# Performance work log

Measured on AMD Instinct MI355X. Metric: run time of the kernel, lower is better.

The kernel has to match this reference:

```python
import jax, jax.numpy as jnp
import numpy as np

B = 256
NUM_ROUTES = 1152
NUM_CAPS = 10
D_IN = 8
D_OUT = 16
NUM_ITER = 3
EPS = 1e-5


def setup_inputs() -> dict:
    key = jax.random.key(0)
    k1, k2 = jax.random.split(key)
    u = jax.random.normal(k1, (B, NUM_ROUTES, D_IN), dtype=jnp.float32)
    # learned transform W, torch shape (1, R, C, D_OUT, D_IN) with leading 1 dropped
    W = jax.random.normal(k2, (NUM_ROUTES, NUM_CAPS, D_OUT, D_IN), dtype=jnp.float32)
    return {"u": u, "W": W}


def _squash(x, eps=EPS):
    # In the original, squash sums over the last dim of s_j, which has size 1,
    # so it is effectively elementwise: scale = x^2/(1+x^2), out = scale*x/(|x|+eps)
    sq = x * x
    return sq / (1.0 + sq) * x / (jnp.sqrt(sq) + eps)


def reference(u, W):
    # u_hat[b,r,c,d] = sum_i W[r,c,d,i] * u[b,r,i]   -> (B, R, C, D_OUT)
    u_hat = jnp.einsum('rcdi,bri->brcd', W, u)
    b_ij = jnp.zeros((1, NUM_ROUTES, NUM_CAPS, 1), dtype=u_hat.dtype)
    v = None
    for it in range(NUM_ITER):
        c_ij = jax.nn.softmax(b_ij, axis=1)              # (1, R, C, K), K in {1, D_OUT}
        s = jnp.sum(c_ij * u_hat, axis=1, keepdims=True)  # (B, 1, C, D_OUT)
        v = _squash(s)
        if it < NUM_ITER - 1:
            # a_ij[b,r,c,d] = v[b,0,c,d] * sum_k u_hat[b,r,c,k]  (exact reduction of
            # the original transpose-multiply-sum, avoiding the DxD intermediate)
            a = v * jnp.sum(u_hat, axis=-1, keepdims=True)  # (B, R, C, D_OUT)
            b_ij = b_ij + jnp.mean(a, axis=0, keepdims=True)
    return v.reshape(u.shape[0], NUM_CAPS, D_OUT)
```

## Files before the change

### kernel.cpp

```cpp
#include <hip/hip_runtime.h>
#include <math.h>

#define R_   1152
#define C_   10
#define D_   16
#define I_   8
#define B_   256
#define N_   160
#define K_   9216
#define KS_  32
#define KC_  288

#define OFF_WSUM  0
#define OFF_TT    92160
#define OFF_V     (OFF_TT + 2949120)
#define OFF_BIJ   (OFF_V + 40960)
#define OFF_E     (OFF_BIJ + 184320)
#define OFF_NSA   (OFF_E + 184320)
#define OFF_NSB   (OFF_NSA + 160)
#define OFF_PART  (OFF_NSB + 160)

__device__ __forceinline__ float f4c(const float4 v, int i) {
    return i == 0 ? v.x : i == 1 ? v.y : i == 2 ? v.z : v.w;
}

template <int HASE>
__launch_bounds__(256, 2)
__global__ void gemm_kernel(const float* __restrict__ u, const float* __restrict__ W,
                            const float* __restrict__ E,
                            float* __restrict__ partials, float* __restrict__ Wsum,
                            float* __restrict__ zA, float* __restrict__ zB) {
    int tid = threadIdx.x;
    if (!HASE && blockIdx.x >= 512) {
        int idx = (blockIdx.x - 512) * 256 + tid;
        int r = idx / (C_ * I_);
        int rem = idx % (C_ * I_);
        int c = rem / I_;
        int i = rem % I_;
        const float* p = W + (size_t)r * (C_ * D_ * I_) + c * (D_ * I_) + i;
        float s = 0.0f;
#pragma unroll
        for (int d = 0; d < D_; ++d) s += p[d * I_];
        Wsum[idx] = s;
        return;
    }

    __shared__ float smem[10240];
    int wave = tid >> 6, lane = tid & 63;
    int ng = lane & 15, bg = lane >> 4;
    int bt = blockIdx.x & 15, ks = blockIdx.x >> 4;
    int b0 = bt * 16;
    int n0 = ng * 10;

    if (!HASE && blockIdx.x == 0 && tid < N_) { zA[tid] = 0.0f; zB[tid] = 0.0f; }

    float acc[4][10];
#pragma unroll
    for (int m = 0; m < 4; ++m)
#pragma unroll
        for (int j = 0; j < 10; ++j) acc[m][j] = 0.0f;

    const float* ubase = u + (size_t)(b0 + bg * 4) * K_ + ks * KC_ + wave * 8;

    float4 wr[5];
    float  ee[5];
    float4 uc[8];
    {
        int r = ks * 36 + wave;
#pragma unroll
        for (int it = 0; it < 5; ++it) {
            int idx = it * 64 + lane;
            wr[it] = *(const float4*)(W + (size_t)r * 1280 + idx * 4);
            if (HASE) ee[it] = E[r * N_ + (idx >> 1)];
        }
#pragma unroll
        for (int m = 0; m < 4; ++m)
#pragma unroll
            for (int g = 0; g < 2; ++g)
                uc[m * 2 + g] = *(const float4*)(ubase + (size_t)m * K_ + g * 4);
    }

    int ldsbase = wave * 1280;
    for (int c = 0; c < 9; ++c) {
#pragma unroll
        for (int it = 0; it < 5; ++it) {
            int idx = it * 64 + lane;
            int n = idx >> 1, ih = (idx & 1) * 4;
            float e = HASE ? ee[it] : 1.0f;
            float* q = &smem[ldsbase + ih * 160 + n];
            q[0]   = wr[it].x * e;
            q[160] = wr[it].y * e;
            q[320] = wr[it].z * e;
            q[480] = wr[it].w * e;
        }
        float4 un[8];
        if (c < 8) {
            int r = ks * 36 + (c + 1) * 4 + wave;
#pragma unroll
            for (int it = 0; it < 5; ++it) {
                int idx = it * 64 + lane;
                wr[it] = *(const float4*)(W + (size_t)r * 1280 + idx * 4);
                if (HASE) ee[it] = E[r * N_ + (idx >> 1)];
            }
#pragma unroll
            for (int m = 0; m < 4; ++m)
#pragma unroll
                for (int g = 0; g < 2; ++g)
                    un[m * 2 + g] = *(const float4*)(ubase + (size_t)m * K_ + (c + 1) * 32 + g * 4);
        }
#pragma unroll
        for (int g = 0; g < 2; ++g) {
#pragma unroll
            for (int t4 = 0; t4 < 4; ++t4) {
                const float* wrow = &smem[ldsbase + (g * 4 + t4) * 160 + n0];
                float w[10];
#pragma unroll
                for (int j = 0; j < 10; j += 2) {
                    float2 ww = *(const float2*)(wrow + j);
                    w[j] = ww.x; w[j + 1] = ww.y;
                }
#pragma unroll
                for (int m = 0; m < 4; ++m) {
                    float uav = f4c(uc[m * 2 + g], t4);
#pragma unroll
                    for (int j = 0; j < 10; ++j)
                        acc[m][j] = fmaf(uav, w[j], acc[m][j]);
                }
            }
        }
        if (c < 8) {
#pragma unroll
            for (int q2 = 0; q2 < 8; ++q2) uc[q2] = un[q2];
        }
    }

    __syncthreads();
#pragma unroll
    for (int m = 0; m < 4; ++m)
#pragma unroll
        for (int j = 0; j < 10; ++j)
            smem[wave * 2560 + (bg * 4 + m) * N_ + n0 + j] = acc[m][j];
    __syncthreads();
    float* outp = partials + (size_t)ks * (B_ * N_) + (size_t)b0 * N_;
    for (int f = tid; f < 2560; f += 256)
        outp[f] = smem[f] + smem[2560 + f] + smem[5120 + f] + smem[7680 + f];
}

template <int DOT>
__global__ void rsv_kernel(const float* __restrict__ partials, float* __restrict__ dst,
                           float scale, const float* __restrict__ nsum,
                           const float* __restrict__ u,
                           const float* __restrict__ Wsum, float* __restrict__ tT) {
    int tid = threadIdx.x;
    if (DOT && blockIdx.x >= 160) {
        for (int idx = (blockIdx.x - 160) * 256 + tid; idx < B_ * R_; idx += 512 * 256) {
            int r = idx % R_;
            int b = idx / R_;
            const float4* up = (const float4*)(u + (size_t)idx * I_);
            float4 a0 = up[0], a1 = up[1];
            const float* wp = Wsum + (size_t)r * (C_ * I_);
            float outv[C_];
#pragma unroll
            for (int c = 0; c < C_; ++c) {
                const float4* w4 = (const float4*)(wp + c * I_);
                float4 w0 = w4[0], w1 = w4[1];
                outv[c] = a0.x * w0.x + a0.y * w0.y + a0.z * w0.z + a0.w * w0.w
                        + a1.x * w1.x + a1.y * w1.y + a1.z * w1.z + a1.w * w1.w;
            }
#pragma unroll
            for (int c = 0; c < C_; ++c)
                tT[((size_t)c * B_ + b) * R_ + r] = outv[c];
        }
        return;
    }
    int g = blockIdx.x * 256 + tid;
    float s = 0.0f;
#pragma unroll
    for (int ks = 0; ks < KS_; ++ks) s += partials[(size_t)ks * (B_ * N_) + g];
    if (nsum) s /= nsum[g % N_];
    else      s *= scale;
    float sq = s * s;
    dst[g] = sq / (1.0f + sq) * s / (sqrtf(sq) + 1e-5f);
}

__launch_bounds__(256)
__global__ void bupd_kernel(const float* __restrict__ v, const float* __restrict__ tT,
                            float* __restrict__ bij, float* __restrict__ E,
                            float* __restrict__ nsum, int accumulate) {
    __shared__ float vs[B_ * 16];
    __shared__ float red[16 * 258];
    __shared__ float exs[4][16];
    int tid = threadIdx.x;
    int c = blockIdx.x % 10;
    int r0 = (blockIdx.x / 10) * 16;
    int rsub = tid & 15, bs = tid >> 4;

    for (int q = tid; q < 1024; q += 256) {
        int b = q >> 2, d4 = q & 3;
        ((float4*)vs)[q] = *(const float4*)(v + (size_t)b * N_ + c * 16 + d4 * 4);
    }
    __syncthreads();

    float acc[16];
#pragma unroll
    for (int d = 0; d < 16; ++d) acc[d] = 0.0f;

    const float* tp = tT + ((size_t)c * B_ + bs) * R_ + r0 + rsub;
#pragma unroll
    for (int bb = 0; bb < 16; ++bb) {
        float tv = tp[(size_t)bb * 16 * R_];
        const float4* vrow = (const float4*)(vs + (bb * 16 + bs) * 16);
        float4 v0 = vrow[0], v1 = vrow[1], v2 = vrow[2], v3 = vrow[3];
        acc[0]  = fmaf(tv, v0.x, acc[0]);  acc[1]  = fmaf(tv, v0.y, acc[1]);
        acc[2]  = fmaf(tv, v0.z, acc[2]);  acc[3]  = fmaf(tv, v0.w, acc[3]);
        acc[4]  = fmaf(tv, v1.x, acc[4]);  acc[5]  = fmaf(tv, v1.y, acc[5]);
        acc[6]  = fmaf(tv, v1.z, acc[6]);  acc[7]  = fmaf(tv, v1.w, acc[7]);
        acc[8]  = fmaf(tv, v2.x, acc[8]);  acc[9]  = fmaf(tv, v2.y, acc[9]);
        acc[10] = fmaf(tv, v2.z, acc[10]); acc[11] = fmaf(tv, v2.w, acc[11]);
        acc[12] = fmaf(tv, v3.x, acc[12]); acc[13] = fmaf(tv, v3.y, acc[13]);
        acc[14] = fmaf(tv, v3.z, acc[14]); acc[15] = fmaf(tv, v3.w, acc[15]);
    }
#pragma unroll
    for (int d = 0; d < 16; ++d) red[d * 258 + tid] = acc[d];
    __syncthreads();

    int d = tid & 15, rr = tid >> 4;
    const float* rp = red + d * 258 + rr;
    float s = 0.0f;
#pragma unroll
    for (int q = 0; q < 16; ++q) s += rp[q * 16];
    s *= (1.0f / B_);
    int o = (r0 + rr) * N_ + c * 16 + d;
    if (accumulate) s += bij[o];
    bij[o] = s;
    float ex = __expf(s);
    E[o] = ex;
    ex += __shfl_down(ex, 32, 64);
    ex += __shfl_down(ex, 16, 64);
    int wv = tid >> 6, ln = tid & 63;
    if (ln < 16) exs[wv][ln] = ex;
    __syncthreads();
    if (tid < 16)
        atomicAdd(&nsum[c * 16 + tid],
                  exs[0][tid] + exs[1][tid] + exs[2][tid] + exs[3][tid]);
}

extern "C" void kernel_launch(void* const* d_in, const int* in_sizes, int n_in,
                              void* d_out, int out_size, void* d_ws, size_t ws_size,
                              hipStream_t stream) {
    (void)in_sizes; (void)n_in; (void)out_size; (void)ws_size;
    const float* u = (const float*)d_in[0];
    const float* W = (const float*)d_in[1];
    float* out = (float*)d_out;
    float* ws = (float*)d_ws;

    float* Wsum     = ws + OFF_WSUM;
    float* tT       = ws + OFF_TT;
    float* v        = ws + OFF_V;
    float* bij      = ws + OFF_BIJ;
    float* E        = ws + OFF_E;
    float* nsumA    = ws + OFF_NSA;
    float* nsumB    = ws + OFF_NSB;
    float* partials = ws + OFF_PART;

    gemm_kernel<0><<<872, 256, 0, stream>>>(u, W, nullptr, partials, Wsum, nsumA, nsumB);
    rsv_kernel<1><<<672, 256, 0, stream>>>(partials, v, 1.0f / 1152.0f, nullptr, u, Wsum, tT);
    bupd_kernel<<<720, 256, 0, stream>>>(v, tT, bij, E, nsumA, 0);

    gemm_kernel<1><<<512, 256, 0, stream>>>(u, W, E, partials, nullptr, nullptr, nullptr);
    rsv_kernel<0><<<160, 256, 0, stream>>>(partials, v, 1.0f, nsumA, nullptr, nullptr, nullptr);
    bupd_kernel<<<720, 256, 0, stream>>>(v, tT, bij, E, nsumB, 1);

    gemm_kernel<1><<<512, 256, 0, stream>>>(u, W, E, partials, nullptr, nullptr, nullptr);
    rsv_kernel<0><<<160, 256, 0, stream>>>(partials, out, 1.0f, nsumB, nullptr, nullptr, nullptr);
}
```

Before: 143.9 us.

## Fuse tT computation into gemm extra blocks and squash reduction into bupd

The Wsum computation and the per-(b,r) dot products that build tT move into the extra blocks of the first gemm kernel, which stage the W sums in shared memory. The separate reduce-squash kernels before each b-update are folded into bupd_kernel: each block reduces the split-K partials and squashes v into LDS itself. The launch count drops from 8 to 6 and the Wsum and v round-trips are removed. In exchange, each of 180 bupd blocks now redundantly reduces 32 partial slices for its capsule, and each block covers 64 routes instead of 16, which lowers the grid size.

```diff
diff --git a/kernel.cpp b/kernel.cpp
--- a/kernel.cpp
+++ b/kernel.cpp
@@ -1,5 +1,6 @@
 #include <hip/hip_runtime.h>
 #include <math.h>
+
 
 #define R_   1152
 #define C_   10
@@ -11,10 +12,8 @@
 #define KS_  32
 #define KC_  288
 
-#define OFF_WSUM  0
-#define OFF_TT    92160
-#define OFF_V     (OFF_TT + 2949120)
-#define OFF_BIJ   (OFF_V + 40960)
+#define OFF_TT    0
+#define OFF_BIJ   2949120
 #define OFF_E     (OFF_BIJ + 184320)
 #define OFF_NSA   (OFF_E + 184320)
 #define OFF_NSB   (OFF_NSA + 160)
@@ -28,24 +27,51 @@
 __launch_bounds__(256, 2)
 __global__ void gemm_kernel(const float* __restrict__ u, const float* __restrict__ W,
                             const float* __restrict__ E,
-                            float* __restrict__ partials, float* __restrict__ Wsum,
+                            float* __restrict__ partials, float* __restrict__ tT,
                             float* __restrict__ zA, float* __restrict__ zB) {
     int tid = threadIdx.x;
+    __shared__ float smem[10240];
+
     if (!HASE && blockIdx.x >= 512) {
-        int idx = (blockIdx.x - 512) * 256 + tid;
-        int r = idx / (C_ * I_);
-        int rem = idx % (C_ * I_);
-        int c = rem / I_;
-        int i = rem % I_;
-        const float* p = W + (size_t)r * (C_ * D_ * I_) + c * (D_ * I_) + i;
-        float s = 0.0f;
-#pragma unroll
-        for (int d = 0; d < D_; ++d) s += p[d * I_];
-        Wsum[idx] = s;
+        float* wsl = smem;
+        int r0 = (int)(blockIdx.x - 512) * 16;
+        for (int q = tid; q < 1280; q += 256) {
+            int rr = q / 80, rem = q % 80;
+            const float* p = W + (size_t)(r0 + rr) * 1280 + (rem >> 3) * 128 + (rem & 7);
+            float s = 0.0f;
+#pragma unroll
+            for (int d = 0; d < 16; ++d) s += p[d * 8];
+            wsl[rr * 84 + rem] = s;
+        }
+        __syncthreads();
+        int r = tid & 15, bgrp = tid >> 4;
+        const float* urow = u + (size_t)(r0 + r) * 8;
+        for (int cb = 0; cb < 4; ++cb) {
+            float4 ua[4][2];
+#pragma unroll
+            for (int b4 = 0; b4 < 4; ++b4) {
+                int b = (cb * 4 + b4) * 16 + bgrp;
+                const float4* up = (const float4*)(urow + (size_t)b * K_);
+                ua[b4][0] = up[0]; ua[b4][1] = up[1];
+            }
+#pragma unroll
+            for (int c = 0; c < 10; ++c) {
+                float4 w0 = *(const float4*)&wsl[r * 84 + c * 8];
+                float4 w1 = *(const float4*)&wsl[r * 84 + c * 8 + 4];
+#pragma unroll
+                for (int b4 = 0; b4 < 4; ++b4) {
+                    int b = (cb * 4 + b4) * 16 + bgrp;
+                    float s = ua[b4][0].x * w0.x + ua[b4][0].y * w0.y
+                            + ua[b4][0].z * w0.z + ua[b4][0].w * w0.w
+                            + ua[b4][1].x * w1.x + ua[b4][1].y * w1.y
+                            + ua[b4][1].z * w1.z + ua[b4][1].w * w1.w;
+                    tT[((size_t)c * B_ + b) * R_ + r0 + r] = s;
+                }
+            }
+        }
         return;
     }
 
-    __shared__ float smem[10240];
     int wave = tid >> 6, lane = tid & 63;
     int ng = lane & 15, bg = lane >> 4;
     int bt = blockIdx.x & 15, ks = blockIdx.x >> 4;
@@ -146,70 +172,44 @@
         outp[f] = smem[f] + smem[2560 + f] + smem[5120 + f] + smem[7680 + f];
 }
 
-template <int DOT>
-__global__ void rsv_kernel(const float* __restrict__ partials, float* __restrict__ dst,
-                           float scale, const float* __restrict__ nsum,
-                           const float* __restrict__ u,
-                           const float* __restrict__ Wsum, float* __restrict__ tT) {
-    int tid = threadIdx.x;
-    if (DOT && blockIdx.x >= 160) {
-        for (int idx = (blockIdx.x - 160) * 256 + tid; idx < B_ * R_; idx += 512 * 256) {
-            int r = idx % R_;
-            int b = idx / R_;
-            const float4* up = (const float4*)(u + (size_t)idx * I_);
-            float4 a0 = up[0], a1 = up[1];
-            const float* wp = Wsum + (size_t)r * (C_ * I_);
-            float outv[C_];
-#pragma unroll
-            for (int c = 0; c < C_; ++c) {
-                const float4* w4 = (const float4*)(wp + c * I_);
-                float4 w0 = w4[0], w1 = w4[1];
-                outv[c] = a0.x * w0.x + a0.y * w0.y + a0.z * w0.z + a0.w * w0.w
-                        + a1.x * w1.x + a1.y * w1.y + a1.z * w1.z + a1.w * w1.w;
-            }
-#pragma unroll
-            for (int c = 0; c < C_; ++c)
-                tT[((size_t)c * B_ + b) * R_ + r] = outv[c];
-        }
-        return;
-    }
-    int g = blockIdx.x * 256 + tid;
-    float s = 0.0f;
-#pragma unroll
-    for (int ks = 0; ks < KS_; ++ks) s += partials[(size_t)ks * (B_ * N_) + g];
-    if (nsum) s /= nsum[g % N_];
-    else      s *= scale;
-    float sq = s * s;
-    dst[g] = sq / (1.0f + sq) * s / (sqrtf(sq) + 1e-5f);
-}
-
 __launch_bounds__(256)
-__global__ void bupd_kernel(const float* __restrict__ v, const float* __restrict__ tT,
+__global__ void bupd_kernel(const float* __restrict__ partials, const float* __restrict__ tT,
                             float* __restrict__ bij, float* __restrict__ E,
-                            float* __restrict__ nsum, int accumulate) {
+                            float* __restrict__ nsumOut, const float* __restrict__ nsumIn,
+                            int accumulate) {
     __shared__ float vs[B_ * 16];
     __shared__ float red[16 * 258];
     __shared__ float exs[4][16];
     int tid = threadIdx.x;
     int c = blockIdx.x % 10;
-    int r0 = (blockIdx.x / 10) * 16;
-    int rsub = tid & 15, bs = tid >> 4;
-
-    for (int q = tid; q < 1024; q += 256) {
-        int b = q >> 2, d4 = q & 3;
-        ((float4*)vs)[q] = *(const float4*)(v + (size_t)b * N_ + c * 16 + d4 * 4);
-    }
-    __syncthreads();
-
+    int r0 = (blockIdx.x / 10) * 64;
+
+    {
+        int d = tid & 15, bq = tid >> 4;
+        const float* pp = partials + c * 16 + d;
+        float inv = accumulate ? 1.0f / nsumIn[c * 16 + d] : (1.0f / 1152.0f);
+        for (int bb = 0; bb < 16; ++bb) {
+            int b = bq * 16 + bb;
+            float s = 0.0f;
+#pragma unroll
+            for (int ks = 0; ks < KS_; ++ks) s += pp[(size_t)ks * (B_ * N_) + b * N_];
+            s *= inv;
+            float sq = s * s;
+            vs[b * 16 + d] = sq / (1.0f + sq) * s / (sqrtf(sq) + 1e-5f);
+        }
+    }
+    __syncthreads();
+
+    int rsub = tid & 63, bs = tid >> 6;
     float acc[16];
 #pragma unroll
     for (int d = 0; d < 16; ++d) acc[d] = 0.0f;
 
-    const float* tp = tT + ((size_t)c * B_ + bs) * R_ + r0 + rsub;
-#pragma unroll
-    for (int bb = 0; bb < 16; ++bb) {
-        float tv = tp[(size_t)bb * 16 * R_];
-        const float4* vrow = (const float4*)(vs + (bb * 16 + bs) * 16);
+    const float* tp = tT + (size_t)c * B_ * R_ + r0 + rsub;
+    for (int bb = 0; bb < 64; ++bb) {
+        int b = bb * 4 + bs;
+        float tv = tp[(size_t)b * R_];
+        const float4* vrow = (const float4*)(vs + b * 16);
         float4 v0 = vrow[0], v1 = vrow[1], v2 = vrow[2], v3 = vrow[3];
         acc[0]  = fmaf(tv, v0.x, acc[0]);  acc[1]  = fmaf(tv, v0.y, acc[1]);
         acc[2]  = fmaf(tv, v0.z, acc[2]);  acc[3]  = fmaf(tv, v0.w, acc[3]);
@@ -224,25 +224,39 @@
     for (int d = 0; d < 16; ++d) red[d * 258 + tid] = acc[d];
     __syncthreads();
 
-    int d = tid & 15, rr = tid >> 4;
-    const float* rp = red + d * 258 + rr;
+    int d2 = tid & 15, rg = tid >> 4;
+    float exacc = 0.0f;
+#pragma unroll
+    for (int j = 0; j < 4; ++j) {
+        int rr = rg + j * 16;
+        const float* rp = red + d2 * 258 + rr;
+        float s = (rp[0] + rp[64] + rp[128] + rp[192]) * (1.0f / B_);
+        int o = (r0 + rr) * N_ + c * 16 + d2;
+        if (accumulate) s += bij[o];
+        bij[o] = s;
+        float ex = __expf(s);
+        E[o] = ex;
+        exacc += ex;
+    }
+    exacc += __shfl_down(exacc, 16, 64);
+    exacc += __shfl_down(exacc, 32, 64);
+    int wv = tid >> 6, ln = tid & 63;
+    if (ln < 16) exs[wv][ln] = exacc;
+    __syncthreads();
+    if (tid < 16)
+        atomicAdd(&nsumOut[c * 16 + tid],
+                  exs[0][tid] + exs[1][tid] + exs[2][tid] + exs[3][tid]);
+}
+
+__global__ void rsv_kernel(const float* __restrict__ partials, float* __restrict__ dst,
+                           const float* __restrict__ nsum) {
+    int g = blockIdx.x * 256 + threadIdx.x;
     float s = 0.0f;
 #pragma unroll
-    for (int q = 0; q < 16; ++q) s += rp[q * 16];
-    s *= (1.0f / B_);
-    int o = (r0 + rr) * N_ + c * 16 + d;
-    if (accumulate) s += bij[o];
-    bij[o] = s;
-    float ex = __expf(s);
-    E[o] = ex;
-    ex += __shfl_down(ex, 32, 64);
-    ex += __shfl_down(ex, 16, 64);
-    int wv = tid >> 6, ln = tid & 63;
-    if (ln < 16) exs[wv][ln] = ex;
-    __syncthreads();
-    if (tid < 16)
-        atomicAdd(&nsum[c * 16 + tid],
-                  exs[0][tid] + exs[1][tid] + exs[2][tid] + exs[3][tid]);
+    for (int ks = 0; ks < KS_; ++ks) s += partials[(size_t)ks * (B_ * N_) + g];
+    s /= nsum[g % N_];
+    float sq = s * s;
+    dst[g] = sq / (1.0f + sq) * s / (sqrtf(sq) + 1e-5f);
 }
 
 extern "C" void kernel_launch(void* const* d_in, const int* in_sizes, int n_in,
@@ -254,23 +268,19 @@
     float* out = (float*)d_out;
     float* ws = (float*)d_ws;
 
-    float* Wsum     = ws + OFF_WSUM;
     float* tT       = ws + OFF_TT;
-    float* v        = ws + OFF_V;
     float* bij      = ws + OFF_BIJ;
     float* E        = ws + OFF_E;
     float* nsumA    = ws + OFF_NSA;
     float* nsumB    = ws + OFF_NSB;
     float* partials = ws + OFF_PART;
 
-    gemm_kernel<0><<<872, 256, 0, stream>>>(u, W, nullptr, partials, Wsum, nsumA, nsumB);
-    rsv_kernel<1><<<672, 256, 0, stream>>>(partials, v, 1.0f / 1152.0f, nullptr, u, Wsum, tT);
-    bupd_kernel<<<720, 256, 0, stream>>>(v, tT, bij, E, nsumA, 0);
+    gemm_kernel<0><<<584, 256, 0, stream>>>(u, W, nullptr, partials, tT, nsumA, nsumB);
+    bupd_kernel<<<180, 256, 0, stream>>>(partials, tT, bij, E, nsumA, nullptr, 0);
 
     gemm_kernel<1><<<512, 256, 0, stream>>>(u, W, E, partials, nullptr, nullptr, nullptr);
-    rsv_kernel<0><<<160, 256, 0, stream>>>(partials, v, 1.0f, nsumA, nullptr, nullptr, nullptr);
-    bupd_kernel<<<720, 256, 0, stream>>>(v, tT, bij, E, nsumB, 1);
+    bupd_kernel<<<180, 256, 0, stream>>>(partials, tT, bij, E, nsumB, nsumA, 1);
 
     gemm_kernel<1><<<512, 256, 0, stream>>>(u, W, E, partials, nullptr, nullptr, nullptr);
-    rsv_kernel<0><<<160, 256, 0, stream>>>(partials, out, 1.0f, nsumB, nullptr, nullptr, nullptr);
-}
+    rsv_kernel<<<160, 256, 0, stream>>>(partials, out, nsumB);
+}
```

Result: slower. 162.8 us (+13.1%).
